# Performance work log

Measured on AMD Instinct MI355X. Metric: run time of the kernel, lower is better.

Reference implementation:

```python
import jax, jax.numpy as jnp
import numpy as np
from jax import lax

D_TEMPORAL, D_INNER, D_STATE, D_CONV, DT_RANK = 2, 4, 16, 4, 1
EPS = 1e-5


def setup_inputs() -> dict:
    key = jax.random.key(0)
    ks = jax.random.split(key, 14)
    B, L = 16, 32768
    f = lambda k, s, scale=1.0: jax.random.normal(k, s, jnp.float32) * scale
    dt_b = float(np.log(np.expm1(0.01)))  # softplus^-1(0.01), typical dt init
    A_log = jnp.log(jnp.tile(jnp.arange(1, D_STATE + 1, dtype=jnp.float32), (D_INNER, 1)))
    return {
        "hidden_states": f(ks[0], (B, D_TEMPORAL, L)),
        "norm_w": jnp.ones((D_TEMPORAL,), jnp.float32),
        "in_proj_w": f(ks[1], (2 * D_INNER, D_TEMPORAL), 0.5),
        "conv_w": f(ks[2], (D_INNER, D_CONV), 0.3),
        "conv_b": f(ks[3], (D_INNER,), 0.1),
        "x_proj_w": f(ks[4], (DT_RANK + 2 * D_STATE, D_INNER), 0.3),
        "dt_proj_w": f(ks[5], (D_INNER, DT_RANK), 1.0),
        "dt_proj_b": jnp.full((D_INNER,), dt_b, jnp.float32),
        "A_log": A_log,
        "D": jnp.ones((D_INNER,), jnp.float32),
        "conv_w_b": f(ks[6], (D_INNER, D_CONV), 0.3),
        "conv_b_b": f(ks[7], (D_INNER,), 0.1),
        "x_proj_w_b": f(ks[8], (DT_RANK + 2 * D_STATE, D_INNER), 0.3),
        "dt_proj_w_b": f(ks[9], (D_INNER, DT_RANK), 1.0),
        "dt_proj_b_b": jnp.full((D_INNER,), dt_b, jnp.float32),
        "A_b_log": A_log,
        "D_b": jnp.ones((D_INNER,), jnp.float32),
        "out_proj_w": f(ks[10], (D_TEMPORAL, D_INNER), 0.3),
        "norm_f_w": jnp.ones((D_TEMPORAL,), jnp.float32),
    }


def _silu(x):
    return x * jax.nn.sigmoid(x)


def _rmsnorm(x, w):
    return x * lax.rsqrt(jnp.mean(x * x, axis=-1, keepdims=True) + EPS) * w


def _branch(x, z, conv_w, conv_b, x_proj_w, dt_proj_w, dt_proj_b, A_log, D):
    # x, z: (B, d_inner, L). Causal depthwise conv + silu.
    Bb, d, L = x.shape
    xc = lax.conv_general_dilated(
        x, conv_w[:, None, :], (1,), [(D_CONV - 1, 0)],
        feature_group_count=d, dimension_numbers=("NCH", "OIH", "NCH"))
    u = _silu(xc + conv_b[None, :, None]).transpose(0, 2, 1)      # (B, L, d)
    x_dbl = u @ x_proj_w.T                                        # (B, L, rank+2n)
    dt, Bm, Cm = jnp.split(x_dbl, [DT_RANK, DT_RANK + D_STATE], axis=-1)
    dt = jax.nn.softplus(dt @ dt_proj_w.T + dt_proj_b)            # (B, L, d)
    A = -jnp.exp(A_log)                                           # (d, n)
    dA = jnp.exp(dt[..., None] * A)                               # (B, L, d, n)
    dBu = (dt * u)[..., None] * Bm[:, :, None, :]                 # (B, L, d, n)

    def step(h, inp):
        dA_t, dBu_t, C_t = inp
        h = dA_t * h + dBu_t                                      # (B, d, n)
        return h, jnp.einsum("bdn,bn->bd", h, C_t)

    h0 = jnp.zeros((Bb, d, D_STATE), dtype=u.dtype)
    _, ys = lax.scan(step, h0, (jnp.swapaxes(dA, 0, 1), jnp.swapaxes(dBu, 0, 1), jnp.swapaxes(Cm, 0, 1)))
    y = jnp.swapaxes(ys, 0, 1) + u * D                            # (B, L, d)
    return y * _silu(z.transpose(0, 2, 1))


def _forward(hidden_states, norm_w, in_proj_w, conv_w, conv_b, x_proj_w, dt_proj_w,
             dt_proj_b, A_log, D, conv_w_b, conv_b_b, x_proj_w_b, dt_proj_w_b,
             dt_proj_b_b, A_b_log, D_b, out_proj_w, norm_f_w):
    # hidden_states: (B, T=d_temporal, L); scan runs over L.
    hs = jnp.swapaxes(hidden_states, 1, 2)                        # (B, L, T)
    residual = hs.astype(jnp.float32)
    hs = _rmsnorm(residual, norm_w)
    xz = jnp.swapaxes(hs @ in_proj_w.T, 1, 2)                     # (B, 2*d_inner, L)
    x, z = jnp.split(xz, 2, axis=1)
    y_f = _branch(x, z, conv_w, conv_b, x_proj_w, dt_proj_w, dt_proj_b, A_log, D)
    y_b = _branch(x[..., ::-1], z[..., ::-1], conv_w_b, conv_b_b, x_proj_w_b,
                  dt_proj_w_b, dt_proj_b_b, A_b_log, D_b)
    y = y_f + y_b[:, ::-1, :]                                     # (B, L, d_inner)
    out = y @ out_proj_w.T                                        # (B, L, T)
    out = _rmsnorm(out + residual, norm_f_w)
    return jnp.swapaxes(out, 1, 2)                                # (B, T, L)


def reference(hidden_states, norm_w, in_proj_w, conv_w, conv_b, x_proj_w, dt_proj_w,
              dt_proj_b, A_log, D, conv_w_b, conv_b_b, x_proj_w_b, dt_proj_w_b,
              dt_proj_b_b, A_b_log, D_b, out_proj_w, norm_f_w):
    return _forward(hidden_states, norm_w, in_proj_w, conv_w, conv_b, x_proj_w,
                    dt_proj_w, dt_proj_b, A_log, D, conv_w_b, conv_b_b, x_proj_w_b,
                    dt_proj_w_b, dt_proj_b_b, A_b_log, D_b, out_proj_w, norm_f_w)
```

## Files before the change

kernel.cpp:

```cpp
#include <hip/hip_runtime.h>
#include <cstdint>

#define BB 16
#define LL 32768
#define NC 512
#define NSPAN 32
#define SPLEN 16

#define WD_SZ 256
#define XPW 0
#define CVW 132
#define CVB 148
#define DTW 152
#define DTB 156
#define AW  160
#define DW  224
#define G_INPROJ 512
#define G_NORMW 528
#define G_OUTP 530
#define G_NORMF 538
#define FLG 1000

#define PQ_OFF 4096
#define PQ_BYTES ((size_t)BB*2*NC*64*8)
#define SP_OFF (PQ_OFF + PQ_BYTES)
#define SP_BYTES ((size_t)BB*2*NSPAN*64*8)
#define WG_OFF (SP_OFF + SP_BYTES)
#define WG_BYTES ((size_t)BB*NC*2*64*64*2)
#define YB_OFF (WG_OFF + WG_BYTES)
#define YB_BYTES ((size_t)BB*NC*64*4*4)

#define LOG2E 1.4426950408889634f

__device__ __forceinline__ float bf2f(unsigned short u){ return __uint_as_float(((unsigned int)u)<<16); }
__device__ __forceinline__ float blo(unsigned int u){ return __uint_as_float(u<<16); }
__device__ __forceinline__ float bhi(unsigned int u){ return __uint_as_float(u & 0xffff0000u); }

__device__ __forceinline__ unsigned int cvtpk(float lo, float hi){
  unsigned int r;
  asm("v_cvt_pk_bf16_f32 %0, %1, %2" : "=v"(r) : "v"(lo), "v"(hi));
  return r;
}
__device__ __forceinline__ unsigned short cvt1(float x){
  return (unsigned short)cvtpk(x, x);
}

__device__ __forceinline__ float siluf(float x){ return x / (1.f + __expf(-x)); }
__device__ __forceinline__ float softplusf_(float x){ return fmaxf(x,0.f) + log1pf(__expf(-fabsf(x))); }

__device__ __forceinline__ float exp2fast(float x){
#if __has_builtin(__builtin_amdgcn_exp2f)
  return __builtin_amdgcn_exp2f(x);
#else
  float r; asm("v_exp_f32 %0, %1\ns_nop 0" : "=v"(r) : "v"(x)); return r;
#endif
}

__device__ __forceinline__ float rowsum16(float x){
  asm("s_nop 1\n\t"
      "v_add_f32_dpp %0, %0, %0 row_ror:1 row_mask:0xf bank_mask:0xf\n\t"
      "s_nop 1\n\t"
      "v_add_f32_dpp %0, %0, %0 row_ror:2 row_mask:0xf bank_mask:0xf\n\t"
      "s_nop 1\n\t"
      "v_add_f32_dpp %0, %0, %0 row_ror:4 row_mask:0xf bank_mask:0xf\n\t"
      "s_nop 1\n\t"
      "v_add_f32_dpp %0, %0, %0 row_ror:8 row_mask:0xf bank_mask:0xf"
      : "+v"(x));
  return x;
}

__device__ __forceinline__ float ldw(const void* p, int i, int isf){
  return isf ? ((const float*)p)[i] : bf2f(((const unsigned short*)p)[i]);
}
__device__ __forceinline__ float2 hid2(const void* hid, int isf, int b, int t){
  if (isf){
    const float* p = (const float*)hid;
    return make_float2(p[(size_t)b*2*LL + t], p[(size_t)b*2*LL + LL + t]);
  }
  const unsigned short* p = (const unsigned short*)hid;
  return make_float2(bf2f(p[(size_t)b*2*LL + t]), bf2f(p[(size_t)b*2*LL + LL + t]));
}
__device__ __forceinline__ float4 xrow(const void* __restrict__ hid, int isf,
                                       const float* __restrict__ W, int b, int t){
  float2 h = hid2(hid, isf, b, t);
  float ms = rsqrtf(0.5f*(h.x*h.x + h.y*h.y) + 1e-5f);
  float v0 = h.x*ms*W[G_NORMW], v1 = h.y*ms*W[G_NORMW+1];
  float4 x;
  x.x = W[G_INPROJ+0]*v0 + W[G_INPROJ+1]*v1;
  x.y = W[G_INPROJ+2]*v0 + W[G_INPROJ+3]*v1;
  x.z = W[G_INPROJ+4]*v0 + W[G_INPROJ+5]*v1;
  x.w = W[G_INPROJ+6]*v0 + W[G_INPROJ+7]*v1;
  return x;
}

__global__ void k_prep(const void* __restrict__ normw, const void* __restrict__ inpj,
    const void* __restrict__ cwf, const void* __restrict__ cbf,
    const void* __restrict__ xpf, const void* __restrict__ dwf,
    const void* __restrict__ dbf, const void* __restrict__ alf,
    const void* __restrict__ ddf,
    const void* __restrict__ cwb, const void* __restrict__ cbb,
    const void* __restrict__ xpb, const void* __restrict__ dwb,
    const void* __restrict__ dbb, const void* __restrict__ alb,
    const void* __restrict__ ddb,
    const void* __restrict__ outp, const void* __restrict__ nfw,
    float* __restrict__ W)
{
  const int isf = (((const unsigned int*)ddf)[0] == 0x3F800000u) ? 1 : 0;
  int t = threadIdx.x;
  for (int i=t;i<132;i+=256){ W[XPW+i]=ldw(xpf,i,isf); W[WD_SZ+XPW+i]=ldw(xpb,i,isf); }
  for (int i=t;i<16;i+=256){ W[CVW+i]=ldw(cwf,i,isf); W[WD_SZ+CVW+i]=ldw(cwb,i,isf); W[G_INPROJ+i]=ldw(inpj,i,isf); }
  for (int i=t;i<4;i+=256){
    W[CVB+i]=ldw(cbf,i,isf); W[WD_SZ+CVB+i]=ldw(cbb,i,isf);
    W[DTW+i]=ldw(dwf,i,isf); W[WD_SZ+DTW+i]=ldw(dwb,i,isf);
    W[DTB+i]=ldw(dbf,i,isf); W[WD_SZ+DTB+i]=ldw(dbb,i,isf);
    W[DW+i] =ldw(ddf,i,isf); W[WD_SZ+DW+i] =ldw(ddb,i,isf);
  }
  for (int i=t;i<64;i+=256){
    W[AW+i]       = -__expf(ldw(alf,i,isf)) * LOG2E;
    W[WD_SZ+AW+i] = -__expf(ldw(alb,i,isf)) * LOG2E;
  }
  for (int i=t;i<8;i+=256) W[G_OUTP+i]=ldw(outp,i,isf);
  for (int i=t;i<2;i+=256){ W[G_NORMW+i]=ldw(normw,i,isf); W[G_NORMF+i]=ldw(nfw,i,isf); }
  if (t==0) W[FLG] = (float)isf;
}

template<int DR>
__device__ __forceinline__ float2 scan_store(const float (* __restrict__ dtPd)[68],
    const unsigned short (* __restrict__ dtud)[68],
    const unsigned int (* __restrict__ bcd)[68],
    float (* __restrict__ ySd)[68],
    unsigned short* __restrict__ wrow,
    float Ax, int d, int n, int dn)
{
  unsigned short* wr   = wrow + dn;
  unsigned short* wrHi = wr + 32*64;
  float P = 1.f, h = 0.f;
  for (int j4=0; j4<16; j4++){
    const int t0 = DR ? 60-4*j4 : 4*j4;
    float4  d4 = *(const float4*)&dtPd[d][t0];
    ushort4 u4 = *(const ushort4*)&dtud[d][t0];
    uint4   c4 = *(const uint4*)&bcd[n][t0];
    float da[4]={d4.x,d4.y,d4.z,d4.w};
    unsigned short ua[4]={u4.x,u4.y,u4.z,u4.w};
    unsigned int ca[4]={c4.x,c4.y,c4.z,c4.w};
    float s[4];
    #pragma unroll
    for (int jr=0; jr<4; jr++){
      const int k  = DR ? 3-jr : jr;
      const int tt = t0 + k;
      float e = exp2fast(Ax*da[k]);
      P *= e;
      float Cf = bhi(ca[k]);
      h = fmaf(e, h, bf2f(ua[k])*blo(ca[k]));
      ((tt < 32) ? wr : wrHi)[(tt & 31)*64] = cvt1(P*Cf);
      s[k] = rowsum16(h*Cf);
    }
    if (n == 0) *(float4*)&ySd[d][t0] = make_float4(s[0],s[1],s[2],s[3]);
  }
  return make_float2(P, h);
}

__global__ __launch_bounds__(128, 4) void k_chunk2(const void* __restrict__ hid,
    const float* __restrict__ W, float2* __restrict__ PQ,
    unsigned short* __restrict__ Wg, float4* __restrict__ YB)
{
  __shared__ __align__(16) char smx[2176];
  __shared__ __align__(16) float dtP[2][4][68];
  __shared__ __align__(16) unsigned short dtuP[2][4][68];
  __shared__ __align__(16) unsigned int BCp[2][16][68];
  __shared__ __align__(16) float uD[2][256];
  float4* xb = (float4*)smx;
  float (*yS)[4][68] = (float (*)[4][68])smx;

  const int tid  = threadIdx.x;
  const int wid  = tid >> 6;
  const int lane = tid & 63;
  const int gid  = blockIdx.x;
  const int c    = gid & (NC-1);
  const int b    = gid >> 9;
  const int isf  = (int)W[FLG];

  if (wid == 0){
    int t = c*64 + lane;
    xb[lane+3] = xrow(hid, isf, W, b, t);
    if (lane < 3){
      int t2 = c*64 - 3 + lane;
      float4 v = make_float4(0.f,0.f,0.f,0.f);
      if (t2 >= 0) v = xrow(hid, isf, W, b, t2);
      xb[lane] = v;
    }
    if (lane >= 61){
      int t3 = c*64 + lane + 3;
      float4 v = make_float4(0.f,0.f,0.f,0.f);
      if (t3 < LL) v = xrow(hid, isf, W, b, t3);
      xb[lane+6] = v;
    }
  }
  __syncthreads();
  {
    const float* Wd = W + wid*WD_SZ;
    float4 a0,a1,a2,a3;
    if (wid == 0){ a0=xb[lane];   a1=xb[lane+1]; a2=xb[lane+2]; a3=xb[lane+3]; }
    else         { a0=xb[lane+6]; a1=xb[lane+5]; a2=xb[lane+4]; a3=xb[lane+3]; }
    float u[4];
    u[0] = siluf(Wd[CVB+0] + Wd[CVW+ 0]*a0.x + Wd[CVW+ 1]*a1.x + Wd[CVW+ 2]*a2.x + Wd[CVW+ 3]*a3.x);
    u[1] = siluf(Wd[CVB+1] + Wd[CVW+ 4]*a0.y + Wd[CVW+ 5]*a1.y + Wd[CVW+ 6]*a2.y + Wd[CVW+ 7]*a3.y);
    u[2] = siluf(Wd[CVB+2] + Wd[CVW+ 8]*a0.z + Wd[CVW+ 9]*a1.z + Wd[CVW+10]*a2.z + Wd[CVW+11]*a3.z);
    u[3] = siluf(Wd[CVB+3] + Wd[CVW+12]*a0.w + Wd[CVW+13]*a1.w + Wd[CVW+14]*a2.w + Wd[CVW+15]*a3.w);
    float dtr = Wd[XPW+0]*u[0] + Wd[XPW+1]*u[1] + Wd[XPW+2]*u[2] + Wd[XPW+3]*u[3];
    float4 ud4;
    #pragma unroll
    for (int d2=0; d2<4; d2++){
      float dt = softplusf_(fmaf(Wd[DTW+d2], dtr, Wd[DTB+d2]));
      dtP[wid][d2][lane]  = dt;
      dtuP[wid][d2][lane] = cvt1(dt*u[d2]);
      ((float*)&ud4)[d2] = u[d2]*Wd[DW+d2];
    }
    *(float4*)&uD[wid][lane*4] = ud4;
    #pragma unroll
    for (int n=0; n<16; n++){
      float Bn = Wd[XPW+(1+n)*4+0]*u[0] + Wd[XPW+(1+n)*4+1]*u[1]
               + Wd[XPW+(1+n)*4+2]*u[2] + Wd[XPW+(1+n)*4+3]*u[3];
      float Cn = Wd[XPW+(17+n)*4+0]*u[0] + Wd[XPW+(17+n)*4+1]*u[1]
               + Wd[XPW+(17+n)*4+2]*u[2] + Wd[XPW+(17+n)*4+3]*u[3];
      BCp[wid][n][lane] = cvtpk(Bn, Cn);
    }
  }
  __syncthreads();

  const int d = lane>>4, n = lane&15;
  const float Ax = W[wid*WD_SZ + AW + d*16 + n];
  unsigned short* wrow = Wg + ((size_t)gid*2 + wid)*64*64;
  float2 pq;
  size_t idx;
  if (wid == 0){
    pq  = scan_store<0>(dtP[0], dtuP[0], BCp[0], yS[0], wrow, Ax, d, n, lane);
    idx = ((size_t)(b*2+0)*NC + c);
  } else {
    pq  = scan_store<1>(dtP[1], dtuP[1], BCp[1], yS[1], wrow, Ax, d, n, lane);
    idx = ((size_t)(b*2+1)*NC + (NC-1-c));
  }
  PQ[idx*64 + lane] = pq;
  __syncthreads();

  if (wid == 0){
    float4 v;
    v.x = yS[0][0][lane] + yS[1][0][lane] + uD[0][lane*4+0] + uD[1][lane*4+0];
    v.y = yS[0][1][lane] + yS[1][1][lane] + uD[0][lane*4+1] + uD[1][lane*4+1];
    v.z = yS[0][2][lane] + yS[1][2][lane] + uD[0][lane*4+2] + uD[1][lane*4+2];
    v.w = yS[0][3][lane] + yS[1][3][lane] + uD[0][lane*4+3] + uD[1][lane*4+3];
    YB[(size_t)gid*64 + lane] = v;
  }
}

__global__ __launch_bounds__(64) void k_spans(const float2* __restrict__ PQ,
                                              float2* __restrict__ SP)
{
  const int blk  = blockIdx.x;
  const int lane = threadIdx.x;
  const int bd   = blk >> 5, span = blk & (NSPAN-1);
  const float2* p = PQ + ((size_t)bd*NC + span*SPLEN)*64 + lane;
  float2 v[SPLEN];
  #pragma unroll
  for (int k=0;k<SPLEN;k++) v[k] = p[k*64];
  float A = 1.f, Bc = 0.f;
  #pragma unroll
  for (int k=0;k<SPLEN;k++){ A *= v[k].x; Bc = fmaf(v[k].x, Bc, v[k].y); }
  SP[((size_t)bd*NSPAN + span)*64 + lane] = make_float2(A,Bc);
}

__device__ __forceinline__ float dot16(uint4 q0, uint4 q1, const float* h){
  float4 h0 = *(const float4*)(h+0),  h1 = *(const float4*)(h+4);
  float4 h2 = *(const float4*)(h+8),  h3 = *(const float4*)(h+12);
  float cacc = 0.f;
  cacc = fmaf(blo(q0.x), h0.x, cacc); cacc = fmaf(bhi(q0.x), h0.y, cacc);
  cacc = fmaf(blo(q0.y), h0.z, cacc); cacc = fmaf(bhi(q0.y), h0.w, cacc);
  cacc = fmaf(blo(q0.z), h1.x, cacc); cacc = fmaf(bhi(q0.z), h1.y, cacc);
  cacc = fmaf(blo(q0.w), h1.z, cacc); cacc = fmaf(bhi(q0.w), h1.w, cacc);
  cacc = fmaf(blo(q1.x), h2.x, cacc); cacc = fmaf(bhi(q1.x), h2.y, cacc);
  cacc = fmaf(blo(q1.y), h2.z, cacc); cacc = fmaf(bhi(q1.y), h2.w, cacc);
  cacc = fmaf(blo(q1.z), h3.x, cacc); cacc = fmaf(bhi(q1.z), h3.y, cacc);
  cacc = fmaf(blo(q1.w), h3.z, cacc); cacc = fmaf(bhi(q1.w), h3.w, cacc);
  return cacc;
}

#define WROW 72
__global__ __launch_bounds__(128, 3) void k_final(const void* __restrict__ hid,
    const float* __restrict__ W, const float2* __restrict__ PQ,
    const float2* __restrict__ SP, const unsigned short* __restrict__ Wg,
    const float4* __restrict__ YB, void* __restrict__ out)
{
  __shared__ float h0s[2][64];
  __shared__ __align__(16) float yC[2][64][4];
  __shared__ __align__(16) unsigned short Wt[2][64][WROW];
  const int tid  = threadIdx.x;
  const int wid  = tid >> 6;
  const int lane = tid & 63;
  const int gid  = blockIdx.x;
  const int c    = gid & (NC-1);
  const int b    = gid >> 9;
  const int isf  = (int)W[FLG];

  const uint4* gsrc = (const uint4*)(Wg + ((size_t)gid*2 + wid)*64*64);
  uint4 st[8];
  #pragma unroll
  for (int i=0;i<8;i++) st[i] = gsrc[i*64 + lane];

  {
    const int p  = wid ? (NC-1-c) : c;
    const int bd = b*2 + wid;
    const int s  = p >> 4, wn = p & 15;
    const float2* SPb = SP + (size_t)bd*NSPAN*64 + lane;
    const float2* PQb = PQ + ((size_t)bd*NC + (p & ~15))*64 + lane;
    float h = 0.f;
    #pragma unroll
    for (int jg=0; jg<4; jg++){
      if (jg*8 < s){
        float2 v[8];
        #pragma unroll
        for (int j=0;j<8;j++){ int jj = jg*8+j; v[j] = SPb[(size_t)(jj<s?jj:0)*64]; }
        #pragma unroll
        for (int j=0;j<8;j++){ int jj = jg*8+j; if (jj<s) h = fmaf(v[j].x, h, v[j].y); }
      }
    }
    #pragma unroll
    for (int jg=0; jg<2; jg++){
      if (jg*8 < wn){
        float2 v[8];
        #pragma unroll
        for (int j=0;j<8;j++){ int jj = jg*8+j; v[j] = PQb[(size_t)(jj<wn?jj:0)*64]; }
        #pragma unroll
        for (int j=0;j<8;j++){ int jj = jg*8+j; if (jj<wn) h = fmaf(v[j].x, h, v[j].y); }
      }
    }
    h0s[wid][lane] = h;
  }

  #pragma unroll
  for (int i=0;i<8;i++){
    int j = i*64 + lane;
    *(uint4*)&Wt[wid][j>>3][(j&7)*8] = st[i];
  }
  __syncthreads();

  {
    uint4 wr_[8];
    #pragma unroll
    for (int q=0;q<8;q++) wr_[q] = *(const uint4*)&Wt[wid][lane][q*8];
    float4 cr;
    #pragma unroll
    for (int d2=0; d2<4; d2++)
      ((float*)&cr)[d2] = dot16(wr_[d2*2], wr_[d2*2+1], &h0s[wid][d2*16]);
    *(float4*)&yC[wid][lane][0] = cr;
  }
  __syncthreads();

  {
    const int t  = lane;
    const int tg = c*64 + t;
    float4 cF = *(const float4*)&yC[0][t][0];
    float4 cB = *(const float4*)&yC[1][t][0];
    float4 yb = YB[(size_t)gid*64 + t];

    float2 r = hid2(hid, isf, b, tg);
    float ms0 = rsqrtf(0.5f*(r.x*r.x + r.y*r.y) + 1e-5f);
    float v0 = r.x*ms0*W[G_NORMW], v1 = r.y*ms0*W[G_NORMW+1];
    float z0 = siluf(W[G_INPROJ+ 8]*v0 + W[G_INPROJ+ 9]*v1);
    float z1 = siluf(W[G_INPROJ+10]*v0 + W[G_INPROJ+11]*v1);
    float z2 = siluf(W[G_INPROJ+12]*v0 + W[G_INPROJ+13]*v1);
    float z3 = siluf(W[G_INPROJ+14]*v0 + W[G_INPROJ+15]*v1);

    float y0 = (yb.x + cF.x + cB.x) * z0;
    float y1 = (yb.y + cF.y + cB.y) * z1;
    float y2 = (yb.z + cF.z + cB.z) * z2;
    float y3 = (yb.w + cF.w + cB.w) * z3;
    float o0 = W[G_OUTP+0]*y0 + W[G_OUTP+1]*y1 + W[G_OUTP+2]*y2 + W[G_OUTP+3]*y3;
    float o1 = W[G_OUTP+4]*y0 + W[G_OUTP+5]*y1 + W[G_OUTP+6]*y2 + W[G_OUTP+7]*y3;
    o0 += r.x;
    o1 += r.y;
    float ms = rsqrtf(0.5f*(o0*o0 + o1*o1) + 1e-5f);
    float e0 = o0*ms*W[G_NORMF], e1 = o1*ms*W[G_NORMF+1];
    size_t i0 = (size_t)b*2*LL + tg, i1 = i0 + LL;
    if (isf){
      if (wid == 0) ((float*)out)[i0] = e0;
      else          ((float*)out)[i1] = e1;
    } else {
      if (wid == 0) ((unsigned short*)out)[i0] = cvt1(e0);
      else          ((unsigned short*)out)[i1] = cvt1(e1);
    }
  }
}

extern "C" void kernel_launch(void* const* d_in, const int* in_sizes, int n_in,
                              void* d_out, int out_size, void* d_ws, size_t ws_size,
                              hipStream_t stream)
{
  (void)in_sizes; (void)n_in; (void)out_size; (void)ws_size;
  const void* hid   = d_in[0];
  const void* normw = d_in[1];
  const void* inpj  = d_in[2];
  const void* cwf   = d_in[3];
  const void* cbf   = d_in[4];
  const void* xpf   = d_in[5];
  const void* dwf   = d_in[6];
  const void* dbf   = d_in[7];
  const void* alf   = d_in[8];
  const void* ddf   = d_in[9];
  const void* cwb   = d_in[10];
  const void* cbb   = d_in[11];
  const void* xpb   = d_in[12];
  const void* dwb   = d_in[13];
  const void* dbb   = d_in[14];
  const void* alb   = d_in[15];
  const void* ddb   = d_in[16];
  const void* outp  = d_in[17];
  const void* nfw   = d_in[18];

  float* W            = (float*)d_ws;
  float2* PQ          = (float2*)((char*)d_ws + PQ_OFF);
  float2* SPt         = (float2*)((char*)d_ws + SP_OFF);
  unsigned short* Wg  = (unsigned short*)((char*)d_ws + WG_OFF);
  float4* YB          = (float4*)((char*)d_ws + YB_OFF);

  k_prep<<<1,256,0,stream>>>(normw, inpj, cwf, cbf, xpf, dwf, dbf, alf, ddf,
                             cwb, cbb, xpb, dwb, dbb, alb, ddb, outp, nfw, W);
  k_chunk2<<<BB*NC, 128, 0, stream>>>(hid, W, PQ, Wg, YB);
  k_spans<<<BB*2*NSPAN, 64, 0, stream>>>(PQ, SPt);
  k_final<<<BB*NC, 128, 0, stream>>>(hid, W, PQ, SPt, Wg, YB, d_out);
}
```

Before: 191.5 us.

## Process eight chunks per block in k_final with a rolling carried state

k_final now handles eight consecutive chunks per block instead of one. Each wave builds the starting scan state once from span and chunk prefixes, then carries it forward chunk by chunk with a single PQ fma, instead of rebuilding the prefix for every chunk. The next chunk's weight tile is prefetched into registers while the current chunk's dot products run. The trade-off is a grid one-eighth the size with a serial eight-step loop per wave, and launch bounds relaxed from 3 to 2, so latency hiding and occupancy drop.

After: 181.5 us. 5.2% less time.

```diff
diff --git a/kernel.cpp b/kernel.cpp
--- a/kernel.cpp
+++ b/kernel.cpp
@@ -6,6 +6,7 @@
 #define NC 512
 #define NSPAN 32
 #define SPLEN 16
+#define CPG 8
 
 #define WD_SZ 256
 #define XPW 0
@@ -284,83 +285,121 @@
   return cacc;
 }
 
+__device__ __forceinline__ float compose_h0(const float2* __restrict__ PQ,
+    const float2* __restrict__ SP, int bd, int p, int lane)
+{
+  const int s  = p >> 4, wn = p & 15;
+  const float2* SPb = SP + (size_t)bd*NSPAN*64 + lane;
+  const float2* PQb = PQ + ((size_t)bd*NC + (p & ~15))*64 + lane;
+  float h = 0.f;
+  #pragma unroll
+  for (int jg=0; jg<4; jg++){
+    if (jg*8 < s){
+      float2 v[8];
+      #pragma unroll
+      for (int j=0;j<8;j++){ int jj = jg*8+j; v[j] = SPb[(size_t)(jj<s?jj:0)*64]; }
+      #pragma unroll
+      for (int j=0;j<8;j++){ int jj = jg*8+j; if (jj<s) h = fmaf(v[j].x, h, v[j].y); }
+    }
+  }
+  #pragma unroll
+  for (int jg=0; jg<2; jg++){
+    if (jg*8 < wn){
+      float2 v[8];
+      #pragma unroll
+      for (int j=0;j<8;j++){ int jj = jg*8+j; v[j] = PQb[(size_t)(jj<wn?jj:0)*64]; }
+      #pragma unroll
+      for (int j=0;j<8;j++){ int jj = jg*8+j; if (jj<wn) h = fmaf(v[j].x, h, v[j].y); }
+    }
+  }
+  return h;
+}
+
 #define WROW 72
-__global__ __launch_bounds__(128, 3) void k_final(const void* __restrict__ hid,
+__global__ __launch_bounds__(128, 2) void k_final(const void* __restrict__ hid,
     const float* __restrict__ W, const float2* __restrict__ PQ,
     const float2* __restrict__ SP, const unsigned short* __restrict__ Wg,
     const float4* __restrict__ YB, void* __restrict__ out)
 {
-  __shared__ float h0s[2][64];
-  __shared__ __align__(16) float yC[2][64][4];
   __shared__ __align__(16) unsigned short Wt[2][64][WROW];
+  __shared__ __align__(16) float yC[2][CPG][64][4];
+  __shared__ __align__(16) float h0s[2][64];
   const int tid  = threadIdx.x;
   const int wid  = tid >> 6;
   const int lane = tid & 63;
-  const int gid  = blockIdx.x;
-  const int c    = gid & (NC-1);
-  const int b    = gid >> 9;
+  const int gb   = blockIdx.x;
+  const int b    = gb >> 6;
+  const int c0   = (gb & 63) * CPG;
   const int isf  = (int)W[FLG];
-
-  const uint4* gsrc = (const uint4*)(Wg + ((size_t)gid*2 + wid)*64*64);
+  const int bd   = b*2 + wid;
+
+  const int i_first = wid ? (CPG-1) : 0;
+  const int c_first = c0 + i_first;
+  const int p_first = wid ? (NC-1-c_first) : c_first;
+
+  const uint4* gt0 = (const uint4*)(Wg + ((size_t)(b*NC + c_first)*2 + wid)*64*64);
   uint4 st[8];
   #pragma unroll
-  for (int i=0;i<8;i++) st[i] = gsrc[i*64 + lane];
-
-  {
-    const int p  = wid ? (NC-1-c) : c;
-    const int bd = b*2 + wid;
-    const int s  = p >> 4, wn = p & 15;
-    const float2* SPb = SP + (size_t)bd*NSPAN*64 + lane;
-    const float2* PQb = PQ + ((size_t)bd*NC + (p & ~15))*64 + lane;
-    float h = 0.f;
-    #pragma unroll
-    for (int jg=0; jg<4; jg++){
-      if (jg*8 < s){
-        float2 v[8];
-        #pragma unroll
-        for (int j=0;j<8;j++){ int jj = jg*8+j; v[j] = SPb[(size_t)(jj<s?jj:0)*64]; }
-        #pragma unroll
-        for (int j=0;j<8;j++){ int jj = jg*8+j; if (jj<s) h = fmaf(v[j].x, h, v[j].y); }
+  for (int k2=0;k2<8;k2++) st[k2] = gt0[k2*64 + lane];
+
+  float h = compose_h0(PQ, SP, bd, p_first, lane);
+
+  #pragma unroll
+  for (int k2=0;k2<8;k2++){
+    int j = k2*64 + lane;
+    *(uint4*)&Wt[wid][j>>3][(j&7)*8] = st[k2];
+  }
+
+  const float2* PQd = PQ + (size_t)bd*NC*64 + lane;
+
+  for (int step=0; step<CPG; ++step){
+    const int i_cur = wid ? (CPG-1-step) : step;
+    const int c_cur = c0 + i_cur;
+    const int hasN  = (step < CPG-1);
+    const int i_nxt = wid ? (i_cur-1) : (i_cur+1);
+
+    uint4 sn[8];
+    if (hasN){
+      const uint4* g2 = (const uint4*)(Wg + ((size_t)(b*NC + c0 + i_nxt)*2 + wid)*64*64);
+      #pragma unroll
+      for (int k2=0;k2<8;k2++) sn[k2] = g2[k2*64 + lane];
+    }
+
+    h0s[wid][lane] = h;
+
+    {
+      uint4 wr_[8];
+      #pragma unroll
+      for (int q=0;q<8;q++) wr_[q] = *(const uint4*)&Wt[wid][lane][q*8];
+      float4 cr;
+      #pragma unroll
+      for (int d2=0; d2<4; d2++)
+        ((float*)&cr)[d2] = dot16(wr_[d2*2], wr_[d2*2+1], &h0s[wid][d2*16]);
+      *(float4*)&yC[wid][i_cur][lane][0] = cr;
+    }
+
+    if (hasN){
+      const int q = wid ? (NC-1-c_cur) : c_cur;
+      float2 pq = PQd[(size_t)q*64];
+      h = fmaf(pq.x, h, pq.y);
+      #pragma unroll
+      for (int k2=0;k2<8;k2++){
+        int j = k2*64 + lane;
+        *(uint4*)&Wt[wid][j>>3][(j&7)*8] = sn[k2];
       }
     }
-    #pragma unroll
-    for (int jg=0; jg<2; jg++){
-      if (jg*8 < wn){
-        float2 v[8];
-        #pragma unroll
-        for (int j=0;j<8;j++){ int jj = jg*8+j; v[j] = PQb[(size_t)(jj<wn?jj:0)*64]; }
-        #pragma unroll
-        for (int j=0;j<8;j++){ int jj = jg*8+j; if (jj<wn) h = fmaf(v[j].x, h, v[j].y); }
-      }
-    }
-    h0s[wid][lane] = h;
-  }
-
-  #pragma unroll
-  for (int i=0;i<8;i++){
-    int j = i*64 + lane;
-    *(uint4*)&Wt[wid][j>>3][(j&7)*8] = st[i];
   }
   __syncthreads();
 
-  {
-    uint4 wr_[8];
-    #pragma unroll
-    for (int q=0;q<8;q++) wr_[q] = *(const uint4*)&Wt[wid][lane][q*8];
-    float4 cr;
-    #pragma unroll
-    for (int d2=0; d2<4; d2++)
-      ((float*)&cr)[d2] = dot16(wr_[d2*2], wr_[d2*2+1], &h0s[wid][d2*16]);
-    *(float4*)&yC[wid][lane][0] = cr;
-  }
-  __syncthreads();
-
-  {
+  #pragma unroll
+  for (int ii=0; ii<CPG/2; ii++){
+    const int i  = wid*(CPG/2) + ii;
+    const int c  = c0 + i;
     const int t  = lane;
     const int tg = c*64 + t;
-    float4 cF = *(const float4*)&yC[0][t][0];
-    float4 cB = *(const float4*)&yC[1][t][0];
-    float4 yb = YB[(size_t)gid*64 + t];
+    float4 cF = *(const float4*)&yC[0][i][t][0];
+    float4 cB = *(const float4*)&yC[1][i][t][0];
+    float4 yb = YB[(size_t)(b*NC + c)*64 + t];
 
     float2 r = hid2(hid, isf, b, tg);
     float ms0 = rsqrtf(0.5f*(r.x*r.x + r.y*r.y) + 1e-5f);
@@ -382,11 +421,11 @@
     float e0 = o0*ms*W[G_NORMF], e1 = o1*ms*W[G_NORMF+1];
     size_t i0 = (size_t)b*2*LL + tg, i1 = i0 + LL;
     if (isf){
-      if (wid == 0) ((float*)out)[i0] = e0;
-      else          ((float*)out)[i1] = e1;
+      ((float*)out)[i0] = e0;
+      ((float*)out)[i1] = e1;
     } else {
-      if (wid == 0) ((unsigned short*)out)[i0] = cvt1(e0);
-      else          ((unsigned short*)out)[i1] = cvt1(e1);
+      ((unsigned short*)out)[i0] = cvt1(e0);
+      ((unsigned short*)out)[i1] = cvt1(e1);
     }
   }
 }
@@ -426,5 +465,5 @@
                              cwb, cbb, xpb, dwb, dbb, alb, ddb, outp, nfw, W);
   k_chunk2<<<BB*NC, 128, 0, stream>>>(hid, W, PQ, Wg, YB);
   k_spans<<<BB*2*NSPAN, 64, 0, stream>>>(PQ, SPt);
-  k_final<<<BB*NC, 128, 0, stream>>>(hid, W, PQ, SPt, Wg, YB, d_out);
-}
+  k_final<<<BB*(NC/CPG), 128, 0, stream>>>(hid, W, PQ, SPt, Wg, YB, d_out);
+}
```
